# Performance work log

Hardware: AMD Instinct MI355X
Metric: run time of the kernel (lower is better)

## Reference

```python
import jax, jax.numpy as jnp
import numpy as np

BLKQ = 64
BLKK = 64
TOPK_RATIO = 0.125


def setup_inputs() -> dict:
    key = jax.random.key(0)
    ks = jax.random.split(key, 4)
    B, L, H, D = 1, 4096, 16, 64
    q = jax.random.normal(ks[0], (B, L, H, D), jnp.float32)
    k = jax.random.normal(ks[1], (B, L, H, D), jnp.float32)
    v = jax.random.normal(ks[2], (B, L, H, D), jnp.float32)
    w_proj = jax.random.normal(ks[3], (D, D), jnp.float32) * 0.02
    b_proj = jnp.zeros((D,), jnp.float32)
    return {"q": q, "k": k, "v": v, "w_proj": w_proj, "b_proj": b_proj}


def _sparse_linear_attn(q, k, v, w_proj, b_proj):
    # q,k,v: (B, L, H, D) -> (B, H, L, D)
    q = jnp.transpose(q, (0, 2, 1, 3))
    k = jnp.transpose(k, (0, 2, 1, 3))
    v = jnp.transpose(v, (0, 2, 1, 3))
    B, H, L, D = q.shape
    M, N = L // BLKQ, L // BLKK  # L chosen divisible by block sizes (no padding)
    T = max(1, int(TOPK_RATIO * N))  # selected key blocks per query block

    qb = q.reshape(B, H, M, BLKQ, D)
    kb = k.reshape(B, H, N, BLKK, D)
    vb = v.reshape(B, H, N, BLKK, D)

    # --- block map: mean-pooled block descriptors, topk key blocks per query block ---
    qm = qb.mean(axis=3)  # (B,H,M,D)
    km = kb.mean(axis=3)  # (B,H,N,D)
    blk_scores = jnp.einsum('bhmd,bhnd->bhmn', qm, km)
    _, lut = jax.lax.top_k(blk_scores, T)  # (B,H,M,T) int32

    # --- gather selected K/V blocks ---
    b_idx = jnp.arange(B)[:, None, None, None]
    h_idx = jnp.arange(H)[None, :, None, None]
    k_sel = kb[b_idx, h_idx, lut]  # (B,H,M,T,BLKK,D)
    v_sel = vb[b_idx, h_idx, lut]  # (B,H,M,T,BLKK,D)

    # --- block-sparse softmax attention over gathered keys only ---
    scale = D ** (-0.5)
    att = jnp.einsum('bhmqd,bhmtkd->bhmqtk', qb, k_sel) * scale
    att = att.reshape(B, H, M, BLKQ, T * BLKK)
    p = jax.nn.softmax(att, axis=-1)
    o_s = jnp.einsum('bhmqn,bhmnd->bhmqd', p, v_sel.reshape(B, H, M, T * BLKK, D))
    o_s = o_s.reshape(B, H, L, D)

    # --- global linear attention with softmax feature map ---
    q_fm = jax.nn.softmax(q, axis=-1)
    k_fm = jax.nn.softmax(k, axis=-1)
    kvsum = jnp.einsum('bhld,bhle->bhde', k_fm, v)  # (B,H,D,D)
    ksum = k_fm.sum(axis=2)  # (B,H,D)
    num = jnp.einsum('bhld,bhde->bhle', q_fm, kvsum)
    den = jnp.einsum('bhld,bhd->bhl', q_fm, ksum)[..., None] + 1e-6
    o_l = num / den
    o_l = jnp.einsum('bhld,ed->bhle', o_l, w_proj) + b_proj  # nn.Linear: x @ W.T + b

    o = o_s + o_l
    return jnp.transpose(o, (0, 2, 1, 3))  # (B, L, H, D)


def reference(q, k, v, w_proj, b_proj):
    return _sparse_linear_attn(q, k, v, w_proj, b_proj)
```

## Files before the change

### kernel.cpp

```cpp
#include <hip/hip_runtime.h>


#define NH   16
#define DH   64
#define NBLK 64
#define TSEL 8

typedef unsigned short u16;
typedef unsigned int   u32;
typedef __attribute__((ext_vector_type(8))) short short8;
typedef __attribute__((ext_vector_type(4))) float f4;
typedef __attribute__((ext_vector_type(4))) u32 u32x4;

#define MFMA_BF16(a, b, c) __builtin_amdgcn_mfma_f32_16x16x32_bf16(a, b, c, 0, 0, 0)

__device__ __forceinline__ u16 f2bf_rne(float f) {
  u32 u = __float_as_uint(f);
  u += 0x7fffu + ((u >> 16) & 1u);
  return (u16)(u >> 16);
}
__device__ __forceinline__ u32 pk2(float a, float b) {
  return (u32)f2bf_rne(a) | ((u32)f2bf_rne(b) << 16);
}
__device__ __forceinline__ float bf2f(u16 u) { return __uint_as_float(((u32)u) << 16); }

__device__ __forceinline__ short8 frag_row(const u16* t, int row, int jblk) {
  return *(const short8*)((const char*)t + row * 128 + ((jblk ^ (row & 7)) * 16));
}

__global__ __launch_bounds__(256) void prep_kernel(const float* __restrict__ k,
                                                   const float* __restrict__ v,
                                                   u16* __restrict__ kT,
                                                   u16* __restrict__ vT,
                                                   float* __restrict__ kvp,
                                                   float* __restrict__ ksp,
                                                   float* __restrict__ kmv) {
  __shared__ __align__(16) char vsl[8192];
  __shared__ __align__(16) char kfm[8192];
  __shared__ float kcol[64 * 65];
  __shared__ float redmx[256];
  __shared__ float redsm[256];
  __shared__ float kmred[256];
  __shared__ float ksred[256];
  __shared__ float mxf[64];
  __shared__ float smi[64];
  int b = blockIdx.x;
  int n = (b >> 3) & 63;
  int h = 2 * (b & 7) + (b >> 9);
  int tid = threadIdx.x;
  int w = tid >> 6, lane = tid & 63;
  int row = lane, qd = w;
  int lq = lane & 15, quad = lane >> 4;

  float kv[16];
  {
    const float* kr = k + (size_t)(n * 64 + row) * 1024 + h * 64 + qd * 16;
#pragma unroll
    for (int c4 = 0; c4 < 4; c4++) {
      float4 a = *(const float4*)(kr + c4 * 4);
      kv[c4 * 4] = a.x; kv[c4 * 4 + 1] = a.y; kv[c4 * 4 + 2] = a.z; kv[c4 * 4 + 3] = a.w;
    }
  }
  {
    char* ktb = (char*)(kT + ((size_t)(h * 64 + n)) * 4096);
    uint4 w0 = make_uint4(pk2(kv[0], kv[1]), pk2(kv[2], kv[3]),
                          pk2(kv[4], kv[5]), pk2(kv[6], kv[7]));
    uint4 w1 = make_uint4(pk2(kv[8], kv[9]), pk2(kv[10], kv[11]),
                          pk2(kv[12], kv[13]), pk2(kv[14], kv[15]));
    *(uint4*)(ktb + row * 128 + (((2 * qd) ^ (row & 7)) * 16)) = w0;
    *(uint4*)(ktb + row * 128 + (((2 * qd + 1) ^ (row & 7)) * 16)) = w1;
  }
  {
#pragma unroll
    for (int j = 0; j < 16; j++) kcol[(qd * 16 + j) * 65 + row] = kv[j];
  }
  {
    float mx = kv[0];
#pragma unroll
    for (int j = 1; j < 16; j++) mx = fmaxf(mx, kv[j]);
    redmx[qd * 64 + row] = mx;
  }
  __syncthreads();
  {
    int c = tid & 63, g = tid >> 6;
    float pk = 0.f;
#pragma unroll
    for (int i = 0; i < 16; i++) pk += kcol[c * 65 + g * 16 + i];
    kmred[g * 64 + c] = pk;
  }
  {
    float mx = fmaxf(fmaxf(redmx[row], redmx[64 + row]),
                     fmaxf(redmx[128 + row], redmx[192 + row]));
    float sm = 0.f;
#pragma unroll
    for (int j = 0; j < 16; j++) sm += __expf(kv[j] - mx);
    redsm[qd * 64 + row] = sm;
  }
  __syncthreads();
  if (tid < 64) {
    kmv[h * 4096 + n * 64 + tid] =
        (kmred[tid] + kmred[64 + tid] + kmred[128 + tid] + kmred[192 + tid]) * (1.0f / 64.0f);
    mxf[tid] = fmaxf(fmaxf(redmx[tid], redmx[64 + tid]),
                     fmaxf(redmx[128 + tid], redmx[192 + tid]));
    smi[tid] = 1.0f / (redsm[tid] + redsm[64 + tid] + redsm[128 + tid] + redsm[192 + tid]);
  }
  __syncthreads();

  {
    int c = lane, g = w;
    float e[16];
#pragma unroll
    for (int i = 0; i < 16; i++) {
      int r = g * 16 + i;
      e[i] = __expf(kcol[c * 65 + r] - mxf[r]) * smi[r];
    }
    uint4 x0 = make_uint4(pk2(e[0], e[1]), pk2(e[2], e[3]),
                          pk2(e[4], e[5]), pk2(e[6], e[7]));
    uint4 x1 = make_uint4(pk2(e[8], e[9]), pk2(e[10], e[11]),
                          pk2(e[12], e[13]), pk2(e[14], e[15]));
    *(uint4*)(kfm + c * 128 + (((2 * g) ^ (c & 7)) * 16)) = x0;
    *(uint4*)(kfm + c * 128 + (((2 * g + 1) ^ (c & 7)) * 16)) = x1;
  }
  {
    int c = lane, g = w;
    const float* vcol = v + (size_t)(n * 64 + g * 16) * 1024 + h * 64 + c;
    float vv[16];
#pragma unroll
    for (int i = 0; i < 16; i++) vv[i] = vcol[(size_t)i * 1024];
    uint4 x0 = make_uint4(pk2(vv[0], vv[1]), pk2(vv[2], vv[3]),
                          pk2(vv[4], vv[5]), pk2(vv[6], vv[7]));
    uint4 x1 = make_uint4(pk2(vv[8], vv[9]), pk2(vv[10], vv[11]),
                          pk2(vv[12], vv[13]), pk2(vv[14], vv[15]));
    *(uint4*)(vsl + c * 128 + (((2 * g) ^ (c & 7)) * 16)) = x0;
    *(uint4*)(vsl + c * 128 + (((2 * g + 1) ^ (c & 7)) * 16)) = x1;
  }
  __syncthreads();

  {
    uint4* vt_out = (uint4*)(vT + ((size_t)(h * 64 + n)) * 4096);
    vt_out[tid] = ((const uint4*)vsl)[tid];
    vt_out[256 + tid] = ((const uint4*)vsl)[256 + tid];
  }
  {
    float ks = 0.f;
    short8 x0 = frag_row((const u16*)kfm, lane, 2 * w);
    short8 x1 = frag_row((const u16*)kfm, lane, 2 * w + 1);
#pragma unroll
    for (int e = 0; e < 8; e++) ks += bf2f((u16)x0[e]) + bf2f((u16)x1[e]);
    ksred[tid] = ks;
  }
  {
    f4 acc[4];
    f4 zz = {0.f, 0.f, 0.f, 0.f};
#pragma unroll
    for (int et = 0; et < 4; et++) acc[et] = zz;
#pragma unroll
    for (int ks2 = 0; ks2 < 2; ks2++) {
      short8 a_ = frag_row((const u16*)kfm, w * 16 + lq, 4 * ks2 + quad);
#pragma unroll
      for (int et = 0; et < 4; et++)
        acc[et] = MFMA_BF16(a_, frag_row((const u16*)vsl, et * 16 + lq, 4 * ks2 + quad), acc[et]);
    }
    float* kvb = kvp + ((size_t)(h * 64 + n)) * 4096;
#pragma unroll
    for (int r = 0; r < 4; r++)
#pragma unroll
      for (int et = 0; et < 4; et++)
        kvb[(w * 16 + quad * 4 + r) * 64 + et * 16 + lq] = acc[et][r];
  }
  __syncthreads();
  if (tid < 64)
    ksp[((size_t)(h * 64 + n)) * 64 + tid] = ksred[tid] + ksred[64 + tid] +
                                             ksred[128 + tid] + ksred[192 + tid];
}

__global__ __launch_bounds__(256) void post_kernel(const float* __restrict__ kvp,
                                                   const float* __restrict__ ksp,
                                                   const float* __restrict__ wgt,
                                                   u16* __restrict__ m2t,
                                                   float* __restrict__ ksum) {
  __shared__ float kr[4][64];
  __shared__ float wl[64 * 65];
  int bx = blockIdx.x, tid = threadIdx.x;
  int h = bx >> 4, dq = bx & 15;
  int j = tid & 63, rr = tid >> 6;

  {
    size_t off = (size_t)(dq * 4 + rr) * 64 + j;
    const float* base = kvp + (size_t)h * 64 * 4096 + off;
    float s0 = 0.f, s1 = 0.f, s2 = 0.f, s3 = 0.f;
#pragma unroll
    for (int n4 = 0; n4 < 16; n4++) {
      s0 += base[(size_t)(n4 * 4 + 0) * 4096];
      s1 += base[(size_t)(n4 * 4 + 1) * 4096];
      s2 += base[(size_t)(n4 * 4 + 2) * 4096];
      s3 += base[(size_t)(n4 * 4 + 3) * 4096];
    }
    kr[rr][j] = (s0 + s1) + (s2 + s3);
  }
#pragma unroll
  for (int i = 0; i < 16; i++) {
    int f = i * 256 + tid;
    wl[(f >> 6) * 65 + (f & 63)] = wgt[f];
  }
  __syncthreads();

  {
    int e = tid & 63, rr2 = tid >> 6;
    float acc = 0.f;
#pragma unroll
    for (int jj = 0; jj < 64; jj++) acc = fmaf(kr[rr2][jj], wl[e * 65 + jj], acc);
    int d = dq * 4 + rr2;
    *(u16*)((char*)m2t + (size_t)h * 8192 + e * 128 +
            (((d >> 3) ^ (e & 7)) * 16) + (d & 7) * 2) = f2bf_rne(acc);
  }
  if (dq == 0 && tid < 64) {
    const float* base = ksp + (size_t)h * 64 * 64 + tid;
    float s = 0.f;
#pragma unroll
    for (int n = 0; n < 64; n++) s += base[(size_t)n * 64];
    ksum[h * 64 + tid] = s;
  }
}

__global__ __launch_bounds__(256, 6) void fused_attn_kernel(const float* __restrict__ q,
                                                            const u16* __restrict__ kT,
                                                            const u16* __restrict__ vT,
                                                            const float* __restrict__ kmv,
                                                            const u16* __restrict__ m2t,
                                                            const float* __restrict__ ksum,
                                                            const float* __restrict__ bproj,
                                                            float* __restrict__ out) {
  __shared__ __align__(16) char smem[24576];
  int b = blockIdx.x;
  int m = (b >> 3) & 63;
  int h = 2 * (b & 7) + (b >> 9);
  int tid = threadIdx.x, w = tid >> 6, lane = tid & 63;
  int lq = lane & 15, quad = lane >> 4;
  char* buf = smem;
  char* p_b = smem + 16384 + w * 2048;
  float* km_s = (float*)smem;
  float* qmp = (float*)(smem + 20480);
  float* qmf = (float*)(smem + 21504);

  {
    int c = tid & 63, g = tid >> 6;
    const float* qcol = q + ((size_t)(m * 64 + g * 16)) * 1024 + h * 64 + c;
    float qp = 0.f;
#pragma unroll
    for (int i = 0; i < 16; i++) qp += qcol[(size_t)i * 1024];
    qmp[g * 64 + c] = qp;
#pragma unroll
    for (int i = 0; i < 16; i++) {
      int idx = i * 256 + tid;
      km_s[(idx >> 6) * 65 + (idx & 63)] = kmv[h * 4096 + idx];
    }
  }
  __syncthreads();
  if (tid < 64) qmf[tid] = qmp[tid] + qmp[64 + tid] + qmp[128 + tid] + qmp[192 + tid];
  __syncthreads();
  int blks[8];
  {
    int n = lane;
    float s = 0.f;
#pragma unroll
    for (int d = 0; d < 64; d++) s += qmf[d] * km_s[n * 65 + d];
    float my = s;
#pragma unroll
    for (int t = 0; t < TSEL; t++) {
      float vv = my; int idx = n;
#pragma unroll
      for (int off = 1; off < 64; off <<= 1) {
        float ov = __shfl_xor(vv, off);
        int oi = __shfl_xor(idx, off);
        if (ov > vv || (ov == vv && oi < idx)) { vv = ov; idx = oi; }
      }
      int sel = __builtin_amdgcn_readfirstlane(idx);
      blks[t] = sel;
      if (n == sel) my = -INFINITY;
    }
  }
  __syncthreads();

  const int qrow = w * 16 + lq;
  const float* qr_g = q + ((size_t)(m * 64 + qrow)) * 1024 + h * 64;
  short8 qf[2];
#pragma unroll
  for (int ks = 0; ks < 2; ks++) {
    const float* gp = qr_g + (4 * ks + quad) * 8;
    float4 a = *(const float4*)gp;
    float4 bb = *(const float4*)(gp + 4);
    u32x4 tt = {pk2(a.x, a.y), pk2(a.z, a.w), pk2(bb.x, bb.y), pk2(bb.z, bb.w)};
    qf[ks] = __builtin_bit_cast(short8, tt);
  }

  {
    const uint4* kt0 = (const uint4*)(kT + ((size_t)(h * 64 + blks[0])) * 4096);
    const uint4* vt0 = (const uint4*)(vT + ((size_t)(h * 64 + blks[0])) * 4096);
    ((uint4*)buf)[tid] = kt0[tid];
    ((uint4*)buf)[256 + tid] = kt0[256 + tid];
    ((uint4*)(buf + 8192))[tid] = vt0[tid];
    ((uint4*)(buf + 8192))[256 + tid] = vt0[256 + tid];
  }
  __syncthreads();

  float mrun = -INFINITY, lrun = 0.f;
  f4 o[4];
  f4 zz = {0.f, 0.f, 0.f, 0.f};
#pragma unroll
  for (int et = 0; et < 4; et++) o[et] = zz;

  const u16* kc = (const u16*)buf;
  const u16* vc = (const u16*)(buf + 8192);

  for (int t = 0; t < 8; t++) {
    uint4 pk0, pk1, pv0, pv1;
    if (t < 7) {
      const uint4* ktn = (const uint4*)(kT + ((size_t)(h * 64 + blks[t + 1])) * 4096);
      const uint4* vtn = (const uint4*)(vT + ((size_t)(h * 64 + blks[t + 1])) * 4096);
      pk0 = ktn[tid]; pk1 = ktn[256 + tid];
      pv0 = vtn[tid]; pv1 = vtn[256 + tid];
    }

    f4 s[4];
#pragma unroll
    for (int kt = 0; kt < 4; kt++) s[kt] = zz;
    __builtin_amdgcn_s_setprio(1);
#pragma unroll
    for (int ks = 0; ks < 2; ks++)
#pragma unroll
      for (int kt = 0; kt < 4; kt++)
        s[kt] = MFMA_BF16(frag_row(kc, kt * 16 + lq, 4 * ks + quad), qf[ks], s[kt]);
    __builtin_amdgcn_s_setprio(0);

    float mp = -INFINITY;
#pragma unroll
    for (int kt = 0; kt < 4; kt++)
#pragma unroll
      for (int r = 0; r < 4; r++) mp = fmaxf(mp, s[kt][r]);
    mp = fmaxf(mp, __shfl_xor(mp, 16));
    mp = fmaxf(mp, __shfl_xor(mp, 32));
    mp *= 0.125f;
    if (__any(mp > mrun)) {
      float mn = fmaxf(mrun, mp);
      float al = __expf(mrun - mn);
      mrun = mn;
      lrun *= al;
#pragma unroll
      for (int et = 0; et < 4; et++)
#pragma unroll
        for (int r = 0; r < 4; r++) o[et][r] *= al;
    }
    float rs_ = 0.f;
#pragma unroll
    for (int kt = 0; kt < 4; kt++) {
      float p0 = __expf(fmaf(s[kt][0], 0.125f, -mrun));
      float p1 = __expf(fmaf(s[kt][1], 0.125f, -mrun));
      float p2 = __expf(fmaf(s[kt][2], 0.125f, -mrun));
      float p3 = __expf(fmaf(s[kt][3], 0.125f, -mrun));
      rs_ += p0 + p1 + p2 + p3;
      u32 lo32 = (__float_as_uint(p0) >> 16) | (__float_as_uint(p1) & 0xffff0000u);
      u32 hi32 = (__float_as_uint(p2) >> 16) | (__float_as_uint(p3) & 0xffff0000u);
      int addr = lq * 128 + (((kt * 2 + (quad >> 1)) ^ (lq & 7)) * 16) + (quad & 1) * 8;
      *(uint2*)(p_b + addr) = make_uint2(lo32, hi32);
    }
    rs_ += __shfl_xor(rs_, 16);
    rs_ += __shfl_xor(rs_, 32);
    lrun += rs_;

    __builtin_amdgcn_s_setprio(1);
#pragma unroll
    for (int ks = 0; ks < 2; ks++) {
      short8 pf = frag_row((const u16*)p_b, lq, 4 * ks + quad);
#pragma unroll
      for (int et = 0; et < 4; et++)
        o[et] = MFMA_BF16(frag_row(vc, et * 16 + lq, 4 * ks + quad), pf, o[et]);
    }
    __builtin_amdgcn_s_setprio(0);

    if (t < 7) {
      __syncthreads();
      ((uint4*)buf)[tid] = pk0;
      ((uint4*)buf)[256 + tid] = pk1;
      ((uint4*)(buf + 8192))[tid] = pv0;
      ((uint4*)(buf + 8192))[256 + tid] = pv1;
      __syncthreads();
    }
  }

  __syncthreads();
  {
    const uint4* src = (const uint4*)((const char*)m2t + (size_t)h * 8192);
    ((uint4*)buf)[tid] = src[tid];
    ((uint4*)buf)[256 + tid] = src[256 + tid];
    if (tid < 64) {
      ((float*)(buf + 8192))[tid] = ksum[h * 64 + tid];
      ((float*)(buf + 8448))[tid] = bproj[tid];
    }
  }
  __syncthreads();
  u16* m2_l = (u16*)buf;
  float* ks_s = (float*)(buf + 8192);
  float* b_s = (float*)(buf + 8448);

  float ev[16];
  float mx = -INFINITY;
#pragma unroll
  for (int c4 = 0; c4 < 4; c4++) {
    float4 a = *(const float4*)(qr_g + quad * 16 + c4 * 4);
    ev[c4 * 4] = a.x; ev[c4 * 4 + 1] = a.y; ev[c4 * 4 + 2] = a.z; ev[c4 * 4 + 3] = a.w;
    mx = fmaxf(mx, fmaxf(fmaxf(a.x, a.y), fmaxf(a.z, a.w)));
  }
  mx = fmaxf(mx, __shfl_xor(mx, 16));
  mx = fmaxf(mx, __shfl_xor(mx, 32));
  float sum = 0.f, eks = 0.f;
#pragma unroll
  for (int j = 0; j < 16; j++) {
    float e = __expf(ev[j] - mx);
    ev[j] = e;
    sum += e;
    eks += e * ks_s[quad * 16 + j];
  }
  sum += __shfl_xor(sum, 16); sum += __shfl_xor(sum, 32);
  eks += __shfl_xor(eks, 16); eks += __shfl_xor(eks, 32);
  float invs = 1.0f / sum;
  float den = fmaf(eks, invs, 1e-6f);
  float scale = invs / den;
  uint4 e0v = make_uint4(pk2(ev[0], ev[1]), pk2(ev[2], ev[3]),
                         pk2(ev[4], ev[5]), pk2(ev[6], ev[7]));
  uint4 e1v = make_uint4(pk2(ev[8], ev[9]), pk2(ev[10], ev[11]),
                         pk2(ev[12], ev[13]), pk2(ev[14], ev[15]));
  *(uint4*)(p_b + lq * 128 + (((2 * quad) ^ (lq & 7)) * 16)) = e0v;
  *(uint4*)(p_b + lq * 128 + (((2 * quad + 1) ^ (lq & 7)) * 16)) = e1v;

  f4 oc[4];
  f4 zz2 = {0.f, 0.f, 0.f, 0.f};
#pragma unroll
  for (int et = 0; et < 4; et++) oc[et] = zz2;
  __builtin_amdgcn_s_setprio(1);
#pragma unroll
  for (int ks2 = 0; ks2 < 2; ks2++) {
    short8 ef = frag_row((const u16*)p_b, lq, 4 * ks2 + quad);
#pragma unroll
    for (int et = 0; et < 4; et++)
      oc[et] = MFMA_BF16(frag_row(m2_l, et * 16 + lq, 4 * ks2 + quad), ef, oc[et]);
  }
  __builtin_amdgcn_s_setprio(0);

  float invl = 1.0f / lrun;
  float* gp = out + ((size_t)(m * 64 + qrow)) * 1024 + h * 64 + quad * 4;
#pragma unroll
  for (int et = 0; et < 4; et++) {
    int e0 = et * 16 + quad * 4;
    float4 ov;
    ov.x = o[et][0] * invl + oc[et][0] * scale + b_s[e0 + 0];
    ov.y = o[et][1] * invl + oc[et][1] * scale + b_s[e0 + 1];
    ov.z = o[et][2] * invl + oc[et][2] * scale + b_s[e0 + 2];
    ov.w = o[et][3] * invl + oc[et][3] * scale + b_s[e0 + 3];
    *(float4*)(gp + et * 16) = ov;
  }
}

extern "C" void kernel_launch(void* const* d_in, const int* in_sizes, int n_in,
                              void* d_out, int out_size, void* d_ws, size_t ws_size,
                              hipStream_t stream) {
  const float* q = (const float*)d_in[0];
  const float* k = (const float*)d_in[1];
  const float* v = (const float*)d_in[2];
  const float* w = (const float*)d_in[3];
  const float* b = (const float*)d_in[4];
  float* out = (float*)d_out;

  u16* kT = (u16*)d_ws;
  u16* vT = kT + 4194304;
  float* kvp = (float*)(vT + 4194304);
  float* ksp = kvp + 4194304;
  float* kmv = ksp + 65536;
  float* ksum = kmv + 65536;
  u16* m2t = (u16*)(ksum + 1024);

  prep_kernel<<<1024, 256, 0, stream>>>(k, v, kT, vT, kvp, ksp, kmv);
  post_kernel<<<256, 256, 0, stream>>>(kvp, ksp, w, m2t, ksum);
  fused_attn_kernel<<<1024, 256, 0, stream>>>(q, kT, vT, kmv, m2t, ksum, b, out);
}
```

Baseline: 134.8 us.

## Double-buffer K/V tiles with async global-to-LDS loads in fused attention

Replaces the register-staged prefetch of the next selected K/V block with direct global_load_lds transfers into a second LDS buffer. The loop now ping-pongs between two buffers with a single barrier per iteration, where before it used two barriers plus an LDS store. This frees the registers that held the prefetched tile and takes the copy through VGPRs out of the inner loop. In exchange, LDS per block grows from 24 KB to 40 KB and the occupancy hint drops from 6 to 4 blocks, so fewer workgroups can hide latency.

Result: faster. 131.9 us (-2.2%).

```diff
diff --git a/kernel.cpp b/kernel.cpp
--- a/kernel.cpp
+++ b/kernel.cpp
@@ -26,6 +26,20 @@
 
 __device__ __forceinline__ short8 frag_row(const u16* t, int row, int jblk) {
   return *(const short8*)((const char*)t + row * 128 + ((jblk ^ (row & 7)) * 16));
+}
+
+__device__ __forceinline__ void gload_lds16(const char* g, char* l) {
+  __builtin_amdgcn_global_load_lds(
+      (const __attribute__((address_space(1))) char*)g,
+      (__attribute__((address_space(3))) char*)l, 16, 0, 0);
+}
+
+__device__ __forceinline__ void stage_async(const char* ktb, const char* vtb,
+                                            char* dst, int w, int lane) {
+  const char* s = ((w & 2) ? vtb : ktb) + (w & 1) * 4096 + lane * 16;
+  char* d = dst + ((w & 2) ? 8192 : 0) + (w & 1) * 4096 + lane * 16;
+#pragma unroll
+  for (int i = 0; i < 4; i++) gload_lds16(s + i * 1024, d + i * 1024);
 }
 
 __global__ __launch_bounds__(256) void prep_kernel(const float* __restrict__ k,
@@ -223,7 +237,7 @@
   }
 }
 
-__global__ __launch_bounds__(256, 6) void fused_attn_kernel(const float* __restrict__ q,
+__global__ __launch_bounds__(256, 4) void fused_attn_kernel(const float* __restrict__ q,
                                                             const u16* __restrict__ kT,
                                                             const u16* __restrict__ vT,
                                                             const float* __restrict__ kmv,
@@ -231,14 +245,15 @@
                                                             const float* __restrict__ ksum,
                                                             const float* __restrict__ bproj,
                                                             float* __restrict__ out) {
-  __shared__ __align__(16) char smem[24576];
+  __shared__ __align__(16) char smem[40960];
   int b = blockIdx.x;
   int m = (b >> 3) & 63;
   int h = 2 * (b & 7) + (b >> 9);
   int tid = threadIdx.x, w = tid >> 6, lane = tid & 63;
   int lq = lane & 15, quad = lane >> 4;
-  char* buf = smem;
-  char* p_b = smem + 16384 + w * 2048;
+  char* bufA = smem;
+  char* bufB = smem + 16384;
+  char* p_b = smem + 32768 + w * 2048;
   float* km_s = (float*)smem;
   float* qmp = (float*)(smem + 20480);
   float* qmf = (float*)(smem + 21504);
@@ -294,14 +309,9 @@
     qf[ks] = __builtin_bit_cast(short8, tt);
   }
 
-  {
-    const uint4* kt0 = (const uint4*)(kT + ((size_t)(h * 64 + blks[0])) * 4096);
-    const uint4* vt0 = (const uint4*)(vT + ((size_t)(h * 64 + blks[0])) * 4096);
-    ((uint4*)buf)[tid] = kt0[tid];
-    ((uint4*)buf)[256 + tid] = kt0[256 + tid];
-    ((uint4*)(buf + 8192))[tid] = vt0[tid];
-    ((uint4*)(buf + 8192))[256 + tid] = vt0[256 + tid];
-  }
+  stage_async((const char*)(kT + ((size_t)(h * 64 + blks[0])) * 4096),
+              (const char*)(vT + ((size_t)(h * 64 + blks[0])) * 4096),
+              bufA, w, lane);
   __syncthreads();
 
   float mrun = -INFINITY, lrun = 0.f;
@@ -310,17 +320,17 @@
 #pragma unroll
   for (int et = 0; et < 4; et++) o[et] = zz;
 
-  const u16* kc = (const u16*)buf;
-  const u16* vc = (const u16*)(buf + 8192);
+  char* cur = bufA;
+  char* nxt = bufB;
 
   for (int t = 0; t < 8; t++) {
-    uint4 pk0, pk1, pv0, pv1;
-    if (t < 7) {
-      const uint4* ktn = (const uint4*)(kT + ((size_t)(h * 64 + blks[t + 1])) * 4096);
-      const uint4* vtn = (const uint4*)(vT + ((size_t)(h * 64 + blks[t + 1])) * 4096);
-      pk0 = ktn[tid]; pk1 = ktn[256 + tid];
-      pv0 = vtn[tid]; pv1 = vtn[256 + tid];
-    }
+    if (t < 7)
+      stage_async((const char*)(kT + ((size_t)(h * 64 + blks[t + 1])) * 4096),
+                  (const char*)(vT + ((size_t)(h * 64 + blks[t + 1])) * 4096),
+                  nxt, w, lane);
+
+    const u16* kc = (const u16*)cur;
+    const u16* vc = (const u16*)(cur + 8192);
 
     f4 s[4];
 #pragma unroll
@@ -378,30 +388,23 @@
     }
     __builtin_amdgcn_s_setprio(0);
 
-    if (t < 7) {
-      __syncthreads();
-      ((uint4*)buf)[tid] = pk0;
-      ((uint4*)buf)[256 + tid] = pk1;
-      ((uint4*)(buf + 8192))[tid] = pv0;
-      ((uint4*)(buf + 8192))[256 + tid] = pv1;
-      __syncthreads();
-    }
-  }
-
-  __syncthreads();
+    __syncthreads();
+    char* tmp = cur; cur = nxt; nxt = tmp;
+  }
+
   {
     const uint4* src = (const uint4*)((const char*)m2t + (size_t)h * 8192);
-    ((uint4*)buf)[tid] = src[tid];
-    ((uint4*)buf)[256 + tid] = src[256 + tid];
+    ((uint4*)smem)[tid] = src[tid];
+    ((uint4*)smem)[256 + tid] = src[256 + tid];
     if (tid < 64) {
-      ((float*)(buf + 8192))[tid] = ksum[h * 64 + tid];
-      ((float*)(buf + 8448))[tid] = bproj[tid];
-    }
-  }
-  __syncthreads();
-  u16* m2_l = (u16*)buf;
-  float* ks_s = (float*)(buf + 8192);
-  float* b_s = (float*)(buf + 8448);
+      ((float*)(smem + 8192))[tid] = ksum[h * 64 + tid];
+      ((float*)(smem + 8448))[tid] = bproj[tid];
+    }
+  }
+  __syncthreads();
+  u16* m2_l = (u16*)smem;
+  float* ks_s = (float*)(smem + 8192);
+  float* b_s = (float*)(smem + 8448);
 
   float ev[16];
   float mx = -INFINITY;
```
